# Kernel optimization log

Hardware: AMD Instinct MI355X
Metric: run time of the kernel (lower is better)

The kernel has to match this reference:

```python
import jax, jax.numpy as jnp
import numpy as np

W = 1024          # hpm.W (Fourier window size)
D = 2 * W         # real-ified dimension
BATCH = 2048
P = 8             # number of previous windows
OMEGA = 50        # sparsity level kept by hard threshold
N_ITERS = 10
L = 1.0           # hpm.L (Lipschitz constant, non-learnable)
CLAMP = 150.0


def setup_inputs() -> dict:
    key = jax.random.key(0)
    k1, k2, k3 = jax.random.split(key, 3)
    x = jax.random.normal(k1, (BATCH, D), jnp.float32)
    prev_windows = jax.random.normal(k2, (P, BATCH, D), jnp.float32)
    # learnable dictionary (Fourier-initialized in the original; random orthogonal-ish here)
    W_d = jax.random.normal(k3, (D, D), jnp.float32) / np.float32(np.sqrt(D))
    # S = I - (1/L) W_d^T W_d, exactly as in __init__
    S = jnp.eye(D, dtype=jnp.float32) - (1.0 / L) * (W_d.T @ W_d)
    lambda2 = jnp.array(1.0, jnp.float32)
    return {"x": x, "prev_windows": prev_windows, "W_d": W_d, "S": S, "lambda2": lambda2}


def _hard_thr(v):
    # keep the OMEGA largest-|.| entries along the last axis, zero the rest
    a = jnp.abs(v)
    kth = jax.lax.top_k(a, OMEGA)[0][..., -1:]  # (batch, 1) threshold
    return jnp.where(a >= kth, v, jnp.zeros_like(v))


def reference(x, prev_windows, W_d, S, lambda2):
    # B = (1/L) W_d x         (batch, D); z vectors kept as (batch, D), last dim == the
    # original dim=-2 since trailing singleton dim is squeezed away.
    B = (1.0 / L) * jnp.einsum('ij,bj->bi', W_d, x)
    z = _hard_thr(B)
    z = _hard_thr(B + jnp.einsum('ij,bj->bi', S, z))

    # attention over previous windows
    s_t = jnp.einsum('ji,bj->bi', W_d, z)                       # W_d^T z : (batch, D)
    s_prev = jnp.einsum('ij,pbj->pbi', W_d, prev_windows)       # (P, batch, D)
    # diagonal of (P,batch,batch) matmul == per-(p,b) dot product; compute it directly
    att = jnp.einsum('pbd,bd->pb', s_prev, s_t)                 # (P, batch)
    att = jax.nn.softmax(att, axis=1)
    pw = jnp.clip(prev_windows, -CLAMP, CLAMP)
    z = lambda2 * jnp.sum(pw * att[..., None], axis=0)          # (batch, D)

    # LIHT iterations; only zs[-1] is used downstream, so carry only the last z
    def step(zc, _):
        zn = _hard_thr(B + jnp.einsum('ij,bj->bi', S, zc))
        return zn, None
    z_last, _ = jax.lax.scan(step, z, None, length=N_ITERS)

    # complex power spectrum: sign flip on imag part does not change the norm
    cpx = z_last.reshape(BATCH, 2, W)
    p = cpx[:, 0, :] ** 2 + cpx[:, 1, :] ** 2                   # (batch, W)
    mD = p.sum(0)                                               # (W,)
    mD_norm = (mD - mD.min()) / (mD.max() - mD.min() + 1e-8)
    return mD_norm, z_last
```

## Files before the change

kernel.cpp:

```cpp
#include <hip/hip_runtime.h>


#define DD 2048
#define NB 2048
#define PLANE ((size_t)1 << 22)
#define ZONE 49152

using short8v  = __attribute__((ext_vector_type(8))) short;
using ushort8v = __attribute__((ext_vector_type(8))) unsigned short;
using ushort4v = __attribute__((ext_vector_type(4))) unsigned short;
using float4v  = __attribute__((ext_vector_type(4))) float;

__device__ __forceinline__ unsigned short f2bf(float f) {
  unsigned u = __float_as_uint(f);
  u = u + 0x7fffu + ((u >> 16) & 1u);
  return (unsigned short)(u >> 16);
}
__device__ __forceinline__ float bf2f(unsigned short h) {
  return __uint_as_float((unsigned)h << 16);
}
__device__ __forceinline__ void gload16(const void* g, void* l) {
  __builtin_amdgcn_global_load_lds((const __attribute__((address_space(1))) void*)g,
                                   (__attribute__((address_space(3))) void*)l,
                                   16, 0, 0);
}

template<int R>
__global__ __launch_bounds__(256)
void conv3T(const float* __restrict__ in, unsigned short* __restrict__ p0,
            unsigned short* __restrict__ p1, unsigned short* __restrict__ p2) {
  __shared__ unsigned short lds3[3][4][R][8];
  const int rt = blockIdx.x, c = blockIdx.y, t = threadIdx.x;
  const int cf = (t & 7) * 4;
  const int g = cf >> 3, e0 = cf & 7;
#pragma unroll
  for (int pass = 0; pass < R / 32; ++pass) {
    const int r = pass * 32 + (t >> 3);
    float4 v = *(const float4*)(in + (size_t)(rt * R + r) * DD + c * 32 + cf);
    float vv[4] = {v.x, v.y, v.z, v.w};
    ushort4v o0, o1, o2;
#pragma unroll
    for (int j = 0; j < 4; ++j) {
      unsigned short a0 = f2bf(vv[j]); float r1 = vv[j] - bf2f(a0);
      unsigned short a1 = f2bf(r1);    float r2 = r1 - bf2f(a1);
      unsigned short a2 = f2bf(r2);
      o0[j] = a0; o1[j] = a1; o2[j] = a2;
    }
    *(ushort4v*)&lds3[0][g][r][e0] = o0;
    *(ushort4v*)&lds3[1][g][r][e0] = o1;
    *(ushort4v*)&lds3[2][g][r][e0] = o2;
  }
  __syncthreads();
  const ushort8v* src = (const ushort8v*)lds3;
  const size_t tb = ((size_t)rt * 64 + c) * (R * 32);
#pragma unroll
  for (int w = 0; w < (3 * R) / 64; ++w) {
    const int idx = w * 256 + t;
    const int p = idx / (4 * R), off = idx % (4 * R);
    unsigned short* dst = (p == 0 ? p0 : p == 1 ? p1 : p2) + tb + (size_t)off * 8;
    *(ushort8v*)dst = src[idx];
  }
}

__global__ __launch_bounds__(256)
void tconv3(const float* __restrict__ in, unsigned short* __restrict__ p0,
            unsigned short* __restrict__ p1, unsigned short* __restrict__ p2) {
  __shared__ unsigned short lds3[3][4][64][8];
  const int nt = blockIdx.x, c = blockIdx.y, t = threadIdx.x;
  const int nf = (t & 15) * 4;
#pragma unroll
  for (int pass = 0; pass < 2; ++pass) {
    const int kr = pass * 16 + (t >> 4);
    float4 v = *(const float4*)(in + (size_t)(c * 32 + kr) * DD + nt * 64 + nf);
    float vv[4] = {v.x, v.y, v.z, v.w};
    const int g = kr >> 3, e = kr & 7;
#pragma unroll
    for (int j = 0; j < 4; ++j) {
      unsigned short a0 = f2bf(vv[j]); float r1 = vv[j] - bf2f(a0);
      unsigned short a1 = f2bf(r1);    float r2 = r1 - bf2f(a1);
      unsigned short a2 = f2bf(r2);
      lds3[0][g][nf + j][e] = a0;
      lds3[1][g][nf + j][e] = a1;
      lds3[2][g][nf + j][e] = a2;
    }
  }
  __syncthreads();
  const ushort8v* src = (const ushort8v*)lds3;
  const size_t tb = ((size_t)nt * 64 + c) * 2048;
#pragma unroll
  for (int w = 0; w < 3; ++w) {
    const int idx = w * 256 + t;
    const int p = idx >> 8, off = idx & 255;
    unsigned short* dst = (p == 0 ? p0 : p == 1 ? p1 : p2) + tb + (size_t)off * 8;
    *(ushort8v*)dst = src[idx];
  }
}

template<int ADD>
__global__ __launch_bounds__(256)
void gemm_bf6(const unsigned short* __restrict__ PA,
              const unsigned short* __restrict__ PB,
              const float* __restrict__ Cadd, float* __restrict__ Cout) {
  __shared__ char lds[3 * ZONE];
  const int tid = threadIdx.x, lane = tid & 63, wid = tid >> 6;

  const int lin = (int)blockIdx.x;
  const int xcd = lin & 7, q = lin >> 3;
  const int mt = (xcd >> 1) * 4 + (q >> 3);
  const int nt = (xcd & 1) * 8 + (q & 7);
  const int m0 = mt * 128, n0 = nt * 128;

  auto stage = [&](char* base, int c) {
    if (wid < 2) {
      const size_t at = ((size_t)mt * 64 + c) * 4096;
#pragma unroll
      for (int i = 0; i < 12; ++i) {
        const int slot = wid * 12 + i, p = slot >> 3, j = slot & 7;
        gload16(PA + p * PLANE + at + j * 512 + lane * 8,
                base + p * 8192 + j * 1024 + lane * 16);
      }
    } else {
#pragma unroll
      for (int i = 0; i < 12; ++i) {
        const int bq = (wid - 2) * 12 + i, p = bq >> 3, r = bq & 7;
        const int sub = r >> 2, j = r & 3;
        const size_t bt = ((size_t)(nt * 2 + sub) * 64 + c) * 2048;
        gload16(PB + p * PLANE + bt + j * 512 + lane * 8,
                base + 24576 + p * 8192 + sub * 4096 + j * 1024 + lane * 16);
      }
    }
  };

  float4v acc[4][4] = {};

  const int rsel = (wid >> 1) * 64;
  const int csel = (wid & 1) * 64;
  const int g16  = lane >> 4;
  const int l15  = lane & 15;
  const int aoff = g16 * 2048 + (rsel + l15) * 16;
  const int boff = 24576 + (csel >> 6) * 4096 + g16 * 1024 + l15 * 16;

  stage(lds, 0);
  stage(lds + ZONE, 1);

  int zc = 0, zs = 2;
  for (int c = 0; c < 64; ++c) {
    if (c < 63) asm volatile("s_waitcnt vmcnt(12)" ::: "memory");
    else        asm volatile("s_waitcnt vmcnt(0)"  ::: "memory");
    __builtin_amdgcn_s_barrier();
    __builtin_amdgcn_sched_barrier(0);

    if (c + 2 < 64) stage(lds + zs * ZONE, c + 2);

    const char* cur = lds + zc * ZONE;
    short8v b0[4], b1[4], b2[4];
#pragma unroll
    for (int ng = 0; ng < 4; ++ng) {
      b0[ng] = *(const short8v*)(cur + boff + 0 * 8192 + ng * 256);
      b1[ng] = *(const short8v*)(cur + boff + 1 * 8192 + ng * 256);
      b2[ng] = *(const short8v*)(cur + boff + 2 * 8192 + ng * 256);
    }
#pragma unroll
    for (int mg = 0; mg < 4; ++mg) {
      const short8v a0 = *(const short8v*)(cur + 0 * 8192 + aoff + mg * 256);
      const short8v a1 = *(const short8v*)(cur + 1 * 8192 + aoff + mg * 256);
      const short8v a2 = *(const short8v*)(cur + 2 * 8192 + aoff + mg * 256);
#pragma unroll
      for (int ng = 0; ng < 4; ++ng) {
        float4v t = acc[mg][ng];
        t = __builtin_amdgcn_mfma_f32_16x16x32_bf16(a0, b0[ng], t, 0, 0, 0);
        t = __builtin_amdgcn_mfma_f32_16x16x32_bf16(a0, b1[ng], t, 0, 0, 0);
        t = __builtin_amdgcn_mfma_f32_16x16x32_bf16(a1, b0[ng], t, 0, 0, 0);
        t = __builtin_amdgcn_mfma_f32_16x16x32_bf16(a1, b1[ng], t, 0, 0, 0);
        t = __builtin_amdgcn_mfma_f32_16x16x32_bf16(a0, b2[ng], t, 0, 0, 0);
        t = __builtin_amdgcn_mfma_f32_16x16x32_bf16(a2, b0[ng], t, 0, 0, 0);
        acc[mg][ng] = t;
      }
    }
    zc = (zc == 2) ? 0 : zc + 1;
    zs = (zs == 2) ? 0 : zs + 1;
  }

  const int row0 = m0 + rsel + g16 * 4;
  const int col0 = n0 + csel + l15;
#pragma unroll
  for (int mg = 0; mg < 4; ++mg)
#pragma unroll
    for (int ng = 0; ng < 4; ++ng)
#pragma unroll
      for (int r = 0; r < 4; ++r) {
        const size_t o = (size_t)(row0 + mg * 16 + r) * DD + col0 + ng * 16;
        float v = acc[mg][ng][r];
        if (ADD) v += Cadd[o];
        Cout[o] = v;
      }
}

template<int HASBASE>
__global__ __launch_bounds__(256)
void spapply_sl(const float* __restrict__ M, const float* __restrict__ baseB,
                float* __restrict__ outF, const unsigned* __restrict__ sidx,
                const float* __restrict__ sval, const int* __restrict__ scnt) {
  const int lane = threadIdx.x & 63, w = threadIdx.x >> 6;
  const int b = blockIdx.y * 4 + w;
  const int col = blockIdx.x * 256 + lane * 4;
  __shared__ unsigned sj[4][64];
  __shared__ float    sv[4][64];
  sj[w][lane] = sidx[b * 64 + lane];
  sv[w][lane] = sval[b * 64 + lane];
  const int nc = scnt[b];
  __syncthreads();

  const size_t ro = (size_t)b * DD + col;
  float4 a;
  if (HASBASE) a = *(const float4*)&baseB[ro];
  else         a = make_float4(0.f, 0.f, 0.f, 0.f);

  const float* Mc = M + col;
  auto ld = [&](int t) -> float4 {
    return *(const float4*)(Mc + (size_t)sj[w][t] * DD);
  };
  auto fma4 = [&](int t, const float4& m) {
    const float v = sv[w][t];
    a.x = fmaf(v, m.x, a.x); a.y = fmaf(v, m.y, a.y);
    a.z = fmaf(v, m.z, a.z); a.w = fmaf(v, m.w, a.w);
  };

  float4 m[8];
  int t = 0;
  if (nc >= 8) {
#pragma unroll
    for (int i = 0; i < 8; ++i) m[i] = ld(i);
    for (; t + 16 <= nc; t += 8) {
#pragma unroll
      for (int i = 0; i < 8; ++i) {
        fma4(t + i, m[i]);
        m[i] = ld(t + 8 + i);
      }
    }
#pragma unroll
    for (int i = 0; i < 8; ++i) fma4(t + i, m[i]);
    t += 8;
  }
  for (; t < nc; ++t) {
    float4 mm = ld(t);
    fma4(t, mm);
  }
  *(float4*)&outF[ro] = a;
}

__global__ __launch_bounds__(64)
void topk_kernel(const float* __restrict__ src, unsigned* __restrict__ sidx,
                 float* __restrict__ sval, int* __restrict__ scnt,
                 float* __restrict__ dense, float* __restrict__ mD,
                 int finalMode) {
  const int b = blockIdx.x;
  const int lane = threadIdx.x;
  const float* row = src + (size_t)b * DD;
  float v[32]; unsigned ab[32];
#pragma unroll
  for (int e4 = 0; e4 < 8; ++e4) {
    float4 t = *(const float4*)&row[e4*256 + lane*4];
    v[e4*4+0]=t.x; v[e4*4+1]=t.y; v[e4*4+2]=t.z; v[e4*4+3]=t.w;
  }
#pragma unroll
  for (int e = 0; e < 32; ++e) ab[e] = __float_as_uint(v[e]) & 0x7fffffffu;

  unsigned mxb = 0;
#pragma unroll
  for (int e = 0; e < 32; ++e) mxb = ab[e] > mxb ? ab[e] : mxb;
  for (int off = 32; off; off >>= 1) {
    unsigned o = (unsigned)__shfl_down((int)mxb, off);
    mxb = o > mxb ? o : mxb;
  }
  mxb = (unsigned)__shfl((int)mxb, 0);
  const int emax = (int)(mxb >> 23);

  int eStar = 0, cntAbove = 0;
  {
    int prevc = 0;
    for (int e = emax; e >= 0; --e) {
      unsigned T = ((unsigned)e) << 23;
      int c = 0;
#pragma unroll
      for (int k = 0; k < 32; ++k) c += (ab[k] >= T) ? 1 : 0;
      for (int off = 32; off; off >>= 1) c += __shfl_down(c, off);
      c = __shfl(c, 0);
      if (c >= 50) { eStar = e; cntAbove = prevc; break; }
      prevc = c;
    }
  }
  unsigned kth = ((unsigned)eStar) << 23;
  int kneed = 50 - cntAbove;

  __shared__ int hist[256];
  __shared__ int sh_sel, sh_kneed;
  for (int p = 0; p < 3; ++p) {
    const unsigned mask = (p==0) ? 0x7F800000u : (p==1) ? 0x7FFF8000u : 0x7FFFFF80u;
    const int sh = (p==0) ? 15 : (p==1) ? 7 : 0;
    for (int t = lane; t < 256; t += 64) hist[t] = 0;
    __syncthreads();
#pragma unroll
    for (int e = 0; e < 32; ++e)
      if ((ab[e] & mask) == kth) atomicAdd(&hist[(ab[e] >> sh) & 0xFF], 1);
    __syncthreads();
    int h0 = hist[lane*4+0], h1 = hist[lane*4+1], h2 = hist[lane*4+2], h3 = hist[lane*4+3];
    int s = h0 + h1 + h2 + h3;
    int x = s;
    for (int off = 1; off < 64; off <<= 1) {
      int y = __shfl_down(x, off);
      if (lane + off < 64) x += y;
    }
    int excl = x - s;
    int c3 = excl + h3, c2 = c3 + h2, c1 = c2 + h1, c0 = c1 + h0;
    if (c0 >= kneed && c1   < kneed) { sh_sel = lane*4+0; sh_kneed = kneed - c1;  }
    if (c1 >= kneed && c2   < kneed) { sh_sel = lane*4+1; sh_kneed = kneed - c2;  }
    if (c2 >= kneed && c3   < kneed) { sh_sel = lane*4+2; sh_kneed = kneed - c3;  }
    if (c3 >= kneed && excl < kneed) { sh_sel = lane*4+3; sh_kneed = kneed - excl;}
    __syncthreads();
    kth |= ((unsigned)sh_sel) << sh;
    kneed = sh_kneed;
    __syncthreads();
  }

  int base = 0;
#pragma unroll
  for (int e4 = 0; e4 < 8; ++e4) {
    float o[4];
#pragma unroll
    for (int qq = 0; qq < 4; ++qq) {
      const int e = e4*4 + qq;
      const bool sel = ab[e] >= kth;
      unsigned long long msk = __ballot(sel);
      int pre = __popcll(msk & ((1ull << lane) - 1ull));
      const unsigned gi = (unsigned)(e4*256 + lane*4 + qq);
      if (sel) {
        int slot = base + pre;
        if (slot < 64) { sidx[b*64+slot] = gi; sval[b*64+slot] = v[e]; }
        if (finalMode) atomicAdd(&mD[gi & 1023u], v[e]*v[e]);
      }
      base += __popcll(msk);
      o[qq] = sel ? v[e] : 0.f;
    }
    if (finalMode) {
      float4 t = {o[0],o[1],o[2],o[3]};
      *(float4*)&dense[(size_t)b*DD + e4*256 + lane*4] = t;
    }
  }
  if (lane == 0) scnt[b] = base < 64 ? base : 64;
}

__global__ __launch_bounds__(256)
void attdot_kernel(const float* __restrict__ prev, const float* __restrict__ U,
                   float* __restrict__ att) {
  const int b = blockIdx.x, p = blockIdx.y, tid = threadIdx.x;
  const float* pr = prev + ((size_t)p*NB + b) * DD;
  const float* u  = U + (size_t)b * DD;
  float s = 0.f;
#pragma unroll
  for (int h = 0; h < 2; ++h) {
    int i = (tid + h*256) * 4;
    float4 a = *(const float4*)&pr[i];
    float4 c = *(const float4*)&u[i];
    s += a.x*c.x + a.y*c.y + a.z*c.z + a.w*c.w;
  }
  for (int off = 32; off; off >>= 1) s += __shfl_down(s, off);
  __shared__ float ps[4];
  if ((tid & 63) == 0) ps[tid >> 6] = s;
  __syncthreads();
  if (tid == 0) att[(size_t)p*NB + b] = ps[0]+ps[1]+ps[2]+ps[3];
}

__global__ __launch_bounds__(256)
void softmax_kernel(const float* __restrict__ att, float* __restrict__ attw) {
  const int p = blockIdx.x, tid = threadIdx.x;
  const float* a = att + (size_t)p*NB;
  float loc[8]; float mx = -3.4e38f;
#pragma unroll
  for (int h = 0; h < 8; ++h) { loc[h] = a[tid + h*256]; mx = fmaxf(mx, loc[h]); }
  for (int off = 32; off; off >>= 1) mx = fmaxf(mx, __shfl_down(mx, off));
  __shared__ float ps[4]; __shared__ float sh_m, sh_s;
  if ((tid & 63) == 0) ps[tid >> 6] = mx;
  __syncthreads();
  if (tid == 0) sh_m = fmaxf(fmaxf(ps[0],ps[1]), fmaxf(ps[2],ps[3]));
  __syncthreads();
  const float m = sh_m;
  float sum = 0.f;
#pragma unroll
  for (int h = 0; h < 8; ++h) sum += expf(loc[h] - m);
  for (int off = 32; off; off >>= 1) sum += __shfl_down(sum, off);
  __syncthreads();
  if ((tid & 63) == 0) ps[tid >> 6] = sum;
  __syncthreads();
  if (tid == 0) sh_s = ps[0]+ps[1]+ps[2]+ps[3];
  __syncthreads();
  const float inv = 1.0f / sh_s;
#pragma unroll
  for (int h = 0; h < 8; ++h) attw[(size_t)p*NB + tid + h*256] = expf(loc[h] - m) * inv;
}

__global__ __launch_bounds__(256)
void zatt_kernel(const float* __restrict__ prev, const float* __restrict__ attw,
                 const float* __restrict__ lam, float* __restrict__ Z) {
  const int b = blockIdx.x, tid = threadIdx.x;
  __shared__ float w[8];
  if (tid < 8) w[tid] = attw[(size_t)tid*NB + b];
  __syncthreads();
  const float l2 = lam[0];
#pragma unroll
  for (int h = 0; h < 2; ++h) {
    int i = (tid + h*256) * 4;
    float4 acc = {0.f,0.f,0.f,0.f};
#pragma unroll
    for (int p = 0; p < 8; ++p) {
      float4 pv = *(const float4*)&prev[((size_t)p*NB + b)*DD + i];
      float wp = w[p];
      acc.x += wp * fminf(fmaxf(pv.x, -150.f), 150.f);
      acc.y += wp * fminf(fmaxf(pv.y, -150.f), 150.f);
      acc.z += wp * fminf(fmaxf(pv.z, -150.f), 150.f);
      acc.w += wp * fminf(fmaxf(pv.w, -150.f), 150.f);
    }
    acc.x *= l2; acc.y *= l2; acc.z *= l2; acc.w *= l2;
    *(float4*)&Z[(size_t)b*DD + i] = acc;
  }
}

__global__ __launch_bounds__(256)
void norm_kernel(float* __restrict__ mD) {
  const int tid = threadIdx.x;
  float v[4]; float mn = 3.4e38f, mx = -3.4e38f;
#pragma unroll
  for (int h = 0; h < 4; ++h) {
    v[h] = mD[tid + h*256];
    mn = fminf(mn, v[h]); mx = fmaxf(mx, v[h]);
  }
  for (int off = 32; off; off >>= 1) {
    mn = fminf(mn, __shfl_down(mn, off));
    mx = fmaxf(mx, __shfl_down(mx, off));
  }
  __shared__ float pmn[4], pmx[4]; __shared__ float smn, smx;
  if ((tid & 63) == 0) { pmn[tid>>6] = mn; pmx[tid>>6] = mx; }
  __syncthreads();
  if (tid == 0) {
    smn = fminf(fminf(pmn[0],pmn[1]), fminf(pmn[2],pmn[3]));
    smx = fmaxf(fmaxf(pmx[0],pmx[1]), fmaxf(pmx[2],pmx[3]));
  }
  __syncthreads();
  const float d = smx - smn + 1e-8f;
#pragma unroll
  for (int h = 0; h < 4; ++h) mD[tid + h*256] = (v[h] - smn) / d;
}

extern "C" void kernel_launch(void* const* d_in, const int* in_sizes, int n_in,
                              void* d_out, int out_size, void* d_ws, size_t ws_size,
                              hipStream_t stream) {
  const float* x    = (const float*)d_in[0];
  const float* prev = (const float*)d_in[1];
  const float* Wd   = (const float*)d_in[2];
  const float* S    = (const float*)d_in[3];
  const float* lam  = (const float*)d_in[4];

  float* out   = (float*)d_out;
  float* mD    = out;
  float* zlast = out + 1024;

  float* B  = (float*)d_ws;
  float* C  = B  + (1u << 22);
  float* X1 = C  + (1u << 22);
  unsigned* sidx = (unsigned*)(X1 + (1u << 22));
  float*    sval = (float*)(sidx + 2048*64);
  int*      scnt = (int*)(sval + 2048*64);
  float*    att  = (float*)(scnt + 2048);
  float*    attw = att + 8*2048;
  unsigned short* PA = (unsigned short*)(attw + 8*2048);
  unsigned short* PB = PA + 3 * PLANE;
  float* U = zlast;

  const dim3 gSp(8, NB / 4);
  const dim3 gA(16, 64);
  const dim3 gB(32, 64);

  conv3T<128><<<gA, 256, 0, stream>>>(x,  PA, PA + PLANE, PA + 2*PLANE);
  conv3T<64> <<<gB, 256, 0, stream>>>(Wd, PB, PB + PLANE, PB + 2*PLANE);
  gemm_bf6<0><<<256, 256, 0, stream>>>(PA, PB, nullptr, B);
  topk_kernel<<<NB, 64, 0, stream>>>(B, sidx, sval, scnt, nullptr, nullptr, 0);
  spapply_sl<1><<<gSp, 256, 0, stream>>>(S, B, C, sidx, sval, scnt);
  topk_kernel<<<NB, 64, 0, stream>>>(C, sidx, sval, scnt, nullptr, nullptr, 0);
  spapply_sl<0><<<gSp, 256, 0, stream>>>(Wd, nullptr, X1, sidx, sval, scnt);
  conv3T<128><<<gA, 256, 0, stream>>>(X1, PA, PA + PLANE, PA + 2*PLANE);
  tconv3<<<gB, 256, 0, stream>>>(Wd, PB, PB + PLANE, PB + 2*PLANE);
  gemm_bf6<0><<<256, 256, 0, stream>>>(PA, PB, nullptr, U);
  attdot_kernel<<<dim3(NB, 8), 256, 0, stream>>>(prev, U, att);
  softmax_kernel<<<8, 256, 0, stream>>>(att, attw);
  zatt_kernel<<<NB, 256, 0, stream>>>(prev, attw, lam, X1);
  conv3T<128><<<gA, 256, 0, stream>>>(X1, PA, PA + PLANE, PA + 2*PLANE);
  conv3T<64> <<<gB, 256, 0, stream>>>(S,  PB, PB + PLANE, PB + 2*PLANE);
  gemm_bf6<1><<<256, 256, 0, stream>>>(PA, PB, B, C);
  topk_kernel<<<NB, 64, 0, stream>>>(C, sidx, sval, scnt, nullptr, nullptr, 0);
  for (int it = 1; it < 10; ++it) {
    spapply_sl<1><<<gSp, 256, 0, stream>>>(S, B, C, sidx, sval, scnt);
    const int fin = (it == 9);
    if (fin) hipMemsetAsync(mD, 0, 1024 * sizeof(float), stream);
    topk_kernel<<<NB, 64, 0, stream>>>(C, sidx, sval, scnt,
                                       fin ? zlast : nullptr,
                                       fin ? mD : nullptr, fin);
  }
  norm_kernel<<<1, 256, 0, stream>>>(mD);
}
```

Baseline: 1.098 ms.

## Double-buffer LDS fragments in registers and shrink GEMM LDS ring to two zones

Restructures the bf16x3 GEMM main loop so each iteration reads the next chunk's A/B fragments from LDS into a second register set while issuing the MFMAs on the current set. The LDS ring drops from three zones to two, and launch bounds now request one block per SIMD budget. The aim is to hide LDS read latency behind MFMA work. In exchange it doubles fragment register use and adds an extra barrier per iteration, with less global-load prefetch depth than the three-zone ring.

New measurement: 2.293 ms. 2.09x slower.

```diff
diff --git a/kernel.cpp b/kernel.cpp
--- a/kernel.cpp
+++ b/kernel.cpp
@@ -96,12 +96,17 @@
   }
 }
 
+struct FragSet {
+  short8v A0[4], A1[4], A2[4];
+  short8v B0[4], B1[4], B2[4];
+};
+
 template<int ADD>
-__global__ __launch_bounds__(256)
+__global__ __launch_bounds__(256, 1)
 void gemm_bf6(const unsigned short* __restrict__ PA,
               const unsigned short* __restrict__ PB,
               const float* __restrict__ Cadd, float* __restrict__ Cout) {
-  __shared__ char lds[3 * ZONE];
+  __shared__ char lds[2 * ZONE];
   const int tid = threadIdx.x, lane = tid & 63, wid = tid >> 6;
 
   const int lin = (int)blockIdx.x;
@@ -140,45 +145,71 @@
   const int aoff = g16 * 2048 + (rsel + l15) * 16;
   const int boff = 24576 + (csel >> 6) * 4096 + g16 * 1024 + l15 * 16;
 
-  stage(lds, 0);
-  stage(lds + ZONE, 1);
-
-  int zc = 0, zs = 2;
-  for (int c = 0; c < 64; ++c) {
-    if (c < 63) asm volatile("s_waitcnt vmcnt(12)" ::: "memory");
-    else        asm volatile("s_waitcnt vmcnt(0)"  ::: "memory");
+  FragSet F0, F1;
+
+  auto readFrags = [&](FragSet& F, const char* z) {
+#pragma unroll
+    for (int mg = 0; mg < 4; ++mg) {
+      F.A0[mg] = *(const short8v*)(z + 0 * 8192 + aoff + mg * 256);
+      F.A1[mg] = *(const short8v*)(z + 1 * 8192 + aoff + mg * 256);
+      F.A2[mg] = *(const short8v*)(z + 2 * 8192 + aoff + mg * 256);
+    }
+#pragma unroll
+    for (int ng = 0; ng < 4; ++ng) {
+      F.B0[ng] = *(const short8v*)(z + boff + 0 * 8192 + ng * 256);
+      F.B1[ng] = *(const short8v*)(z + boff + 1 * 8192 + ng * 256);
+      F.B2[ng] = *(const short8v*)(z + boff + 2 * 8192 + ng * 256);
+    }
+  };
+
+  auto mfmaAll = [&](const FragSet& F) {
+#pragma unroll
+    for (int mg = 0; mg < 4; ++mg)
+#pragma unroll
+      for (int ng = 0; ng < 4; ++ng) {
+        float4v t = acc[mg][ng];
+        t = __builtin_amdgcn_mfma_f32_16x16x32_bf16(F.A0[mg], F.B0[ng], t, 0, 0, 0);
+        t = __builtin_amdgcn_mfma_f32_16x16x32_bf16(F.A0[mg], F.B1[ng], t, 0, 0, 0);
+        t = __builtin_amdgcn_mfma_f32_16x16x32_bf16(F.A1[mg], F.B0[ng], t, 0, 0, 0);
+        t = __builtin_amdgcn_mfma_f32_16x16x32_bf16(F.A1[mg], F.B1[ng], t, 0, 0, 0);
+        t = __builtin_amdgcn_mfma_f32_16x16x32_bf16(F.A0[mg], F.B2[ng], t, 0, 0, 0);
+        t = __builtin_amdgcn_mfma_f32_16x16x32_bf16(F.A2[mg], F.B0[ng], t, 0, 0, 0);
+        acc[mg][ng] = t;
+      }
+  };
+
+  char* const z0 = lds;
+  char* const z1 = lds + ZONE;
+
+  stage(z0, 0);
+  stage(z1, 1);
+  asm volatile("s_waitcnt vmcnt(12)" ::: "memory");
+  __builtin_amdgcn_s_barrier();
+  __builtin_amdgcn_sched_barrier(0);
+  readFrags(F0, z0);
+  asm volatile("s_waitcnt lgkmcnt(0)" ::: "memory");
+  __builtin_amdgcn_sched_barrier(0);
+
+  auto iter = [&](int c, FragSet& Fc, FragSet& Fn, char* zc_, char* zn_) {
     __builtin_amdgcn_s_barrier();
     __builtin_amdgcn_sched_barrier(0);
-
-    if (c + 2 < 64) stage(lds + zs * ZONE, c + 2);
-
-    const char* cur = lds + zc * ZONE;
-    short8v b0[4], b1[4], b2[4];
-#pragma unroll
-    for (int ng = 0; ng < 4; ++ng) {
-      b0[ng] = *(const short8v*)(cur + boff + 0 * 8192 + ng * 256);
-      b1[ng] = *(const short8v*)(cur + boff + 1 * 8192 + ng * 256);
-      b2[ng] = *(const short8v*)(cur + boff + 2 * 8192 + ng * 256);
-    }
-#pragma unroll
-    for (int mg = 0; mg < 4; ++mg) {
-      const short8v a0 = *(const short8v*)(cur + 0 * 8192 + aoff + mg * 256);
-      const short8v a1 = *(const short8v*)(cur + 1 * 8192 + aoff + mg * 256);
-      const short8v a2 = *(const short8v*)(cur + 2 * 8192 + aoff + mg * 256);
-#pragma unroll
-      for (int ng = 0; ng < 4; ++ng) {
-        float4v t = acc[mg][ng];
-        t = __builtin_amdgcn_mfma_f32_16x16x32_bf16(a0, b0[ng], t, 0, 0, 0);
-        t = __builtin_amdgcn_mfma_f32_16x16x32_bf16(a0, b1[ng], t, 0, 0, 0);
-        t = __builtin_amdgcn_mfma_f32_16x16x32_bf16(a1, b0[ng], t, 0, 0, 0);
-        t = __builtin_amdgcn_mfma_f32_16x16x32_bf16(a1, b1[ng], t, 0, 0, 0);
-        t = __builtin_amdgcn_mfma_f32_16x16x32_bf16(a0, b2[ng], t, 0, 0, 0);
-        t = __builtin_amdgcn_mfma_f32_16x16x32_bf16(a2, b0[ng], t, 0, 0, 0);
-        acc[mg][ng] = t;
-      }
-    }
-    zc = (zc == 2) ? 0 : zc + 1;
-    zs = (zs == 2) ? 0 : zs + 1;
+    if (c + 2 < 64) {
+      stage(zc_, c + 2);
+      asm volatile("s_waitcnt vmcnt(12)" ::: "memory");
+    } else if (c + 1 < 64) {
+      asm volatile("s_waitcnt vmcnt(0)" ::: "memory");
+    }
+    __builtin_amdgcn_s_barrier();
+    __builtin_amdgcn_sched_barrier(0);
+    if (c + 1 < 64) readFrags(Fn, zn_);
+    mfmaAll(Fc);
+    asm volatile("s_waitcnt lgkmcnt(0)" ::: "memory");
+    __builtin_amdgcn_sched_barrier(0);
+  };
+
+  for (int c = 0; c < 64; c += 2) {
+    iter(c,     F0, F1, z0, z1);
+    iter(c + 1, F1, F0, z1, z0);
   }
 
   const int row0 = m0 + rsel + g16 * 4;
```
